# Kernel optimization log

Measured on AMD Instinct MI355X. Metric: run time of the kernel, lower is better.

## Reference

```python
import jax, jax.numpy as jnp
import numpy as np

N_LOW, N_HIGH = 5000, 50000
E_LH, E_HH = 200000, 400000


def _gatv2(xs, xd, src, dst, Wl, bl, Wr, br, att, bias, n_dst):
    """PyG GATv2Conv with aggr='mean', concat heads. att: [H, C]."""
    H, C = att.shape
    hl = (xs @ Wl + bl).reshape(-1, H, C)   # source transform (messages)
    hr = (xd @ Wr + br).reshape(-1, H, C)   # target transform
    z = jax.nn.leaky_relu(hl[src] + hr[dst], 0.2)        # [E, H, C]
    logit = jnp.einsum('ehc,hc->eh', z, att)             # [E, H]
    m = jax.lax.stop_gradient(jax.ops.segment_max(logit, dst, num_segments=n_dst))
    ex = jnp.exp(logit - m[dst])
    s = jax.ops.segment_sum(ex, dst, num_segments=n_dst)
    alpha = ex / (s[dst] + 1e-16)                        # edge softmax per dst, per head
    msg = hl[src] * alpha[..., None]                     # [E, H, C]
    out = jax.ops.segment_sum(msg, dst, num_segments=n_dst)
    cnt = jax.ops.segment_sum(jnp.ones(dst.shape, xs.dtype), dst, num_segments=n_dst)
    out = out / jnp.maximum(cnt, 1.0)[:, None, None]     # aggr='mean'
    return out.reshape(n_dst, H * C) + bias


def _bn(x, g, b):
    mu = x.mean(0)
    var = x.var(0)
    return (x - mu) * jax.lax.rsqrt(var + 1e-5) * g + b


def setup_inputs() -> dict:
    key = jax.random.key(0)
    it = iter(jax.random.split(key, 64))
    def nk():
        return next(it)
    def glorot(shape):
        s = np.sqrt(2.0 / (shape[0] + shape[-1])).astype(np.float32)
        return jax.random.normal(nk(), shape, jnp.float32) * s
    inp = {}
    inp['xl'] = jax.random.normal(nk(), (N_LOW, 125), jnp.float32)
    inp['xh'] = jax.random.normal(nk(), (N_HIGH, 1), jnp.float32)
    inp['zstd'] = jax.random.normal(nk(), (N_HIGH, 1), jnp.float32)
    inp['si_lh'] = jax.random.randint(nk(), (E_LH,), 0, N_LOW, jnp.int32)
    inp['di_lh'] = jax.random.randint(nk(), (E_LH,), 0, N_HIGH, jnp.int32)
    inp['si_hh'] = jax.random.randint(nk(), (E_HH,), 0, N_HIGH, jnp.int32)
    inp['di_hh'] = jax.random.randint(nk(), (E_HH,), 0, N_HIGH, jnp.int32)
    def gat(pfx, fs, fd, H, C):
        inp[pfx + '_Wl'] = glorot((fs, H * C)); inp[pfx + '_bl'] = jnp.zeros((H * C,), jnp.float32)
        inp[pfx + '_Wr'] = glorot((fd, H * C)); inp[pfx + '_br'] = jnp.zeros((H * C,), jnp.float32)
        inp[pfx + '_att'] = glorot((H, C)); inp[pfx + '_b'] = jnp.zeros((H * C,), jnp.float32)
    gat('d', 125, 1, 1, 256)
    gat('p1', 257, 257, 4, 64)
    gat('p2', 256, 256, 4, 64)
    gat('p3', 256, 256, 1, 64)
    for pfx, dim in [('bn0', 257), ('bn1', 256), ('bn2', 256), ('bn3', 64)]:
        inp[pfx + '_g'] = jnp.ones((dim,), jnp.float32)
        inp[pfx + '_b'] = jnp.zeros((dim,), jnp.float32)
    inp['pr_W1'] = glorot((64, 64)); inp['pr_b1'] = jnp.zeros((64,), jnp.float32)
    inp['pr_W2'] = glorot((64, 1)); inp['pr_b2'] = jnp.zeros((1,), jnp.float32)
    return inp


def reference(xl, xh, zstd, si_lh, di_lh, si_hh, di_hh,
              d_Wl, d_bl, d_Wr, d_br, d_att, d_b,
              p1_Wl, p1_bl, p1_Wr, p1_br, p1_att, p1_b,
              p2_Wl, p2_bl, p2_Wr, p2_br, p2_att, p2_b,
              p3_Wl, p3_bl, p3_Wr, p3_br, p3_att, p3_b,
              bn0_g, bn0_b, bn1_g, bn1_b, bn2_g, bn2_b, bn3_g, bn3_b,
              pr_W1, pr_b1, pr_W2, pr_b2):
    n_high = xh.shape[0]
    # downscaler: bipartite GATv2 (low -> high), heads=1, no self loops
    enc = _gatv2(xl, xh, si_lh, di_lh, d_Wl, d_bl, d_Wr, d_br, d_att, d_b, n_high)
    x = jnp.concatenate([zstd, enc], axis=-1)            # [N_HIGH, 257]
    # high-within-high edges with self loops (add_self_loops=True)
    loop = jnp.arange(n_high, dtype=si_hh.dtype)
    src = jnp.concatenate([si_hh, loop])
    dst = jnp.concatenate([di_hh, loop])
    x = _bn(x, bn0_g, bn0_b)
    x = _gatv2(x, x, src, dst, p1_Wl, p1_bl, p1_Wr, p1_br, p1_att, p1_b, n_high)
    x = jax.nn.relu(_bn(x, bn1_g, bn1_b))
    x = _gatv2(x, x, src, dst, p2_Wl, p2_bl, p2_Wr, p2_br, p2_att, p2_b, n_high)
    x = jax.nn.relu(_bn(x, bn2_g, bn2_b))
    x = _gatv2(x, x, src, dst, p3_Wl, p3_bl, p3_Wr, p3_br, p3_att, p3_b, n_high)
    x = jax.nn.relu(_bn(x, bn3_g, bn3_b))
    # predictor MLP
    y = jax.nn.relu(x @ pr_W1 + pr_b1) @ pr_W2 + pr_b2   # [N_HIGH, 1]
    return y
```

## Files before the change

kernel.cpp:

```cpp
#include <hip/hip_runtime.h>
#include <math.h>

#define DEV __device__ __forceinline__

static const int N_LOW = 5000, N_HIGH = 50000, E_LH = 200000, E_HH = 400000;
static const int E2 = E_HH + N_HIGH;
static const int ETOT = E_LH + E2;
static const int RBLK = 2048;

typedef __attribute__((ext_vector_type(8))) short bf16x8;
typedef __attribute__((ext_vector_type(4))) float f32x4;
typedef __attribute__((ext_vector_type(8))) unsigned short u16x8;
typedef unsigned short u16;

DEV short f2bf(float v) {
    unsigned u = __float_as_uint(v);
    u += 0x7FFFu + ((u >> 16) & 1u);
    return (short)(u >> 16);
}
DEV float bf2f(u16 u) { return __uint_as_float(((unsigned)u) << 16); }

template <int VPL> struct RawTT { using T = u16; };
template <> struct RawTT<4> { using T = ushort4; };

template <bool RELU, bool BF16OUT, bool WIDE>
DEV void gemm_body(const bf16x8* __restrict__ Af, const bf16x8* __restrict__ Bf,
                   const float* __restrict__ bias, float* __restrict__ C,
                   int M, int N, int nkt) {
    const int l = threadIdx.x & 63;
    const int w = threadIdx.x >> 6;
    const int nt0 = WIDE ? w * 4 : blockIdx.x * 4;
    const int mt0 = WIDE ? blockIdx.y * 2 : blockIdx.y * 8 + w * 2;
    f32x4 acc[2][4];
#pragma unroll
    for (int i = 0; i < 2; i++)
#pragma unroll
        for (int j = 0; j < 4; j++) acc[i][j] = (f32x4){0.f, 0.f, 0.f, 0.f};
    const bf16x8* a0p = Af + (size_t)mt0 * nkt * 64 + l;
    const bf16x8* a1p = a0p + (size_t)nkt * 64;
    const bf16x8* bp = Bf + (size_t)nt0 * nkt * 64 + l;
    for (int kt = 0; kt < nkt; kt++) {
        bf16x8 a0 = a0p[kt * 64];
        bf16x8 a1 = a1p[kt * 64];
        bf16x8 b0 = bp[kt * 64];
        bf16x8 b1 = bp[(size_t)(nkt + kt) * 64];
        bf16x8 b2 = bp[(size_t)(2 * nkt + kt) * 64];
        bf16x8 b3 = bp[(size_t)(3 * nkt + kt) * 64];
        acc[0][0] = __builtin_amdgcn_mfma_f32_16x16x32_bf16(a0, b0, acc[0][0], 0, 0, 0);
        acc[0][1] = __builtin_amdgcn_mfma_f32_16x16x32_bf16(a0, b1, acc[0][1], 0, 0, 0);
        acc[0][2] = __builtin_amdgcn_mfma_f32_16x16x32_bf16(a0, b2, acc[0][2], 0, 0, 0);
        acc[0][3] = __builtin_amdgcn_mfma_f32_16x16x32_bf16(a0, b3, acc[0][3], 0, 0, 0);
        acc[1][0] = __builtin_amdgcn_mfma_f32_16x16x32_bf16(a1, b0, acc[1][0], 0, 0, 0);
        acc[1][1] = __builtin_amdgcn_mfma_f32_16x16x32_bf16(a1, b1, acc[1][1], 0, 0, 0);
        acc[1][2] = __builtin_amdgcn_mfma_f32_16x16x32_bf16(a1, b2, acc[1][2], 0, 0, 0);
        acc[1][3] = __builtin_amdgcn_mfma_f32_16x16x32_bf16(a1, b3, acc[1][3], 0, 0, 0);
    }
    const int colb = nt0 * 16 + (l & 15);
    const int rsub = (l >> 4) * 4;
#pragma unroll
    for (int mi = 0; mi < 2; mi++) {
        int rowb = (mt0 + mi) * 16 + rsub;
#pragma unroll
        for (int r = 0; r < 4; r++) {
            int row = rowb + r;
            if (row >= M) continue;
#pragma unroll
            for (int n = 0; n < 4; n++) {
                int col = colb + n * 16;
                float v = acc[mi][n][r] + bias[col];
                if (RELU) v = fmaxf(v, 0.f);
                if (BF16OUT)
                    ((u16*)C)[(size_t)row * N + col] = (u16)f2bf(v);
                else
                    C[(size_t)row * N + col] = v;
            }
        }
    }
}

template <bool RELU, bool BF16OUT, bool WIDE>
__global__ __launch_bounds__(256) void gemm_mfma(
    const bf16x8* __restrict__ Af, const bf16x8* __restrict__ Bf,
    const float* __restrict__ bias, float* __restrict__ C,
    int M, int N, int nkt) {
    gemm_body<RELU, BF16OUT, WIDE>(Af, Bf, bias, C, M, N, nkt);
}

template <bool WIDE>
__global__ __launch_bounds__(256) void gemm_mfma2(
    const bf16x8* __restrict__ Af,
    const bf16x8* __restrict__ Bf0, const bf16x8* __restrict__ Bf1,
    const float* __restrict__ bias0, const float* __restrict__ bias1,
    float* __restrict__ C0, float* __restrict__ C1,
    int M, int N, int nkt) {
    if (blockIdx.z == 0)
        gemm_body<false, true, WIDE>(Af, Bf0, bias0, C0, M, N, nkt);
    else
        gemm_body<false, true, WIDE>(Af, Bf1, bias1, C1, M, N, nkt);
}

template <bool RELU>
__global__ __launch_bounds__(256) void bn_frag(
    const u16* __restrict__ x, int Nrows, int F, int STR, int SS,
    const float* __restrict__ sums,
    const float* __restrict__ g, const float* __restrict__ b,
    bf16x8* __restrict__ Af, int nmt, int nkt) {
    int total = nmt * nkt * 64;
    for (int idx = blockIdx.x * blockDim.x + threadIdx.x; idx < total;
         idx += gridDim.x * blockDim.x) {
        int mt = idx / (nkt * 64);
        int rem = idx - mt * (nkt * 64);
        int kt = rem >> 6, l = rem & 63;
        int row = mt * 16 + (l & 15);
        int colb = kt * 32 + (l >> 4) * 8;
        bf16x8 o;
#pragma unroll
        for (int j = 0; j < 8; j++) {
            int col = colb + j;
            float v = 0.f;
            if (row < Nrows && col < F) {
                float mu = sums[col] / Nrows;
                float var = sums[SS + col] / Nrows - mu * mu;
                float istd = rsqrtf(fmaxf(var, 0.f) + 1e-5f);
                v = (bf2f(x[(size_t)row * STR + col]) - mu) * istd * g[col] + b[col];
                if (RELU) v = fmaxf(v, 0.f);
            }
            o[j] = f2bf(v);
        }
        Af[idx] = o;
    }
}

__global__ __launch_bounds__(256) void cast_frag(
    const float* __restrict__ x, int Nrows, int F,
    bf16x8* __restrict__ Af, int nmt, int nkt) {
    int total = nmt * nkt * 64;
    for (int idx = blockIdx.x * blockDim.x + threadIdx.x; idx < total;
         idx += gridDim.x * blockDim.x) {
        int mt = idx / (nkt * 64);
        int rem = idx - mt * (nkt * 64);
        int kt = rem >> 6, l = rem & 63;
        int row = mt * 16 + (l & 15);
        int colb = kt * 32 + (l >> 4) * 8;
        bf16x8 o;
#pragma unroll
        for (int j = 0; j < 8; j++) {
            int col = colb + j;
            o[j] = (row < Nrows && col < F) ? f2bf(x[(size_t)row * F + col]) : (short)0;
        }
        Af[idx] = o;
    }
}

struct WtJobs {
    const float* W[8];
    bf16x8* out[8];
    int K[8], Nn[8], nnt[8], nkt[8];
};
__global__ __launch_bounds__(256) void wt_frag_all(WtJobs jobs) {
    const int job = blockIdx.y;
    const float* W = jobs.W[job];
    bf16x8* Bf = jobs.out[job];
    const int K = jobs.K[job], N = jobs.Nn[job];
    const int nkt = jobs.nkt[job];
    int total = jobs.nnt[job] * nkt * 64;
    for (int idx = blockIdx.x * blockDim.x + threadIdx.x; idx < total;
         idx += gridDim.x * blockDim.x) {
        int nt = idx / (nkt * 64);
        int rem = idx - nt * (nkt * 64);
        int kt = rem >> 6, l = rem & 63;
        int col = nt * 16 + (l & 15);
        int kb = kt * 32 + (l >> 4) * 8;
        bf16x8 o;
#pragma unroll
        for (int j = 0; j < 8; j++) {
            int k = kb + j;
            o[j] = (k < K && col < N) ? f2bf(W[(size_t)k * N + col]) : (short)0;
        }
        Bf[idx] = o;
    }
}

__global__ __launch_bounds__(256) void hist_all(
    const int* __restrict__ di_lh, const int* __restrict__ di_hh,
    int* __restrict__ cnt) {
    for (int i = blockIdx.x * blockDim.x + threadIdx.x; i < ETOT;
         i += gridDim.x * blockDim.x) {
        if (i < E_LH) {
            atomicAdd(&cnt[di_lh[i]], 1);
        } else {
            int j = i - E_LH;
            int d = (j < E_HH) ? di_hh[j] : (j - E_HH);
            atomicAdd(&cnt[N_HIGH + d], 1);
        }
    }
}

__global__ __launch_bounds__(256) void scan_partial(
    const int* __restrict__ cnt, int* __restrict__ off,
    int* __restrict__ bsum, int n) {
    __shared__ int s[256];
    const int t = threadIdx.x;
    const int base = blockIdx.x * 1024 + t * 4;
    int v0 = (base < n) ? cnt[base] : 0;
    int v1 = (base + 1 < n) ? cnt[base + 1] : 0;
    int v2 = (base + 2 < n) ? cnt[base + 2] : 0;
    int v3 = (base + 3 < n) ? cnt[base + 3] : 0;
    int tsum = v0 + v1 + v2 + v3;
    s[t] = tsum;
    __syncthreads();
    for (int step = 1; step < 256; step <<= 1) {
        int q = (t >= step) ? s[t - step] : 0;
        __syncthreads();
        s[t] += q;
        __syncthreads();
    }
    int excl = s[t] - tsum;
    if (base < n) off[base] = excl;
    if (base + 1 < n) off[base + 1] = excl + v0;
    if (base + 2 < n) off[base + 2] = excl + v0 + v1;
    if (base + 3 < n) off[base + 3] = excl + v0 + v1 + v2;
    if (t == 255) bsum[blockIdx.x] = s[255];
}

__global__ __launch_bounds__(256) void scan_bsums(
    int* __restrict__ bsum, int nb, int* __restrict__ off, int n) {
    __shared__ int s[256];
    const int t = threadIdx.x;
    int v = (t < nb) ? bsum[t] : 0;
    s[t] = v;
    __syncthreads();
    for (int step = 1; step < 256; step <<= 1) {
        int q = (t >= step) ? s[t - step] : 0;
        __syncthreads();
        s[t] += q;
        __syncthreads();
    }
    if (t < nb) bsum[t] = s[t] - v;
    if (t == 255) off[n] = s[255];
}

__global__ __launch_bounds__(256) void scan_add(
    int* __restrict__ off, const int* __restrict__ bsum, int n) {
    int b = blockIdx.x;
    int add = bsum[b];
    int base = b * 1024;
    int end = base + 1024 < n ? base + 1024 : n;
    for (int i = base + threadIdx.x; i < end; i += 256) off[i] += add;
}

__global__ __launch_bounds__(256) void scatter_all(
    const int* __restrict__ si_lh, const int* __restrict__ di_lh,
    const int* __restrict__ si_hh, const int* __restrict__ di_hh,
    int* __restrict__ cur, int* __restrict__ csr) {
    for (int i = blockIdx.x * blockDim.x + threadIdx.x; i < ETOT;
         i += gridDim.x * blockDim.x) {
        int d, s, bucket;
        if (i < E_LH) {
            d = di_lh[i]; s = si_lh[i]; bucket = d;
        } else {
            int j = i - E_LH;
            if (j < E_HH) { d = di_hh[j]; s = si_hh[j]; }
            else { d = s = j - E_HH; }
            bucket = N_HIGH + d;
        }
        int p = atomicAdd(&cur[bucket], 1);
        csr[p] = s;
    }
}

template <int H, int C, bool HR_ONFLY>
__global__ __launch_bounds__(256) void gat_gather(
    const u16* __restrict__ hl, const u16* __restrict__ hr,
    const float* __restrict__ xh, const float* __restrict__ Wr,
    const float* __restrict__ br,
    const int* __restrict__ rowptr, const int* __restrict__ csr_src,
    const float* __restrict__ att, const float* __restrict__ bias,
    u16* __restrict__ out, int outStride, int outOfs, int Ndst,
    const float* __restrict__ col0) {
    constexpr int HC = H * C;
    constexpr int VPL = HC / 64;
    constexpr int LPH = C / VPL;
    using RawT = typename RawTT<VPL>::T;
    int w = blockIdx.x * (blockDim.x >> 6) + (threadIdx.x >> 6);
    if (w >= Ndst) return;
    const int l = threadIdx.x & 63;

    float hrv[VPL], attv[VPL];
    if constexpr (HR_ONFLY) {
        static_assert(!HR_ONFLY || VPL == 4, "onfly assumes VPL==4");
        float xv = xh[w];
        float4 wr = *reinterpret_cast<const float4*>(Wr + l * 4);
        float4 bb = *reinterpret_cast<const float4*>(br + l * 4);
        hrv[0] = fmaf(xv, wr.x, bb.x); hrv[1] = fmaf(xv, wr.y, bb.y);
        hrv[2] = fmaf(xv, wr.z, bb.z); hrv[3] = fmaf(xv, wr.w, bb.w);
        float4 u = *reinterpret_cast<const float4*>(att + l * 4);
        attv[0] = u.x; attv[1] = u.y; attv[2] = u.z; attv[3] = u.w;
    } else if constexpr (VPL == 4) {
        ushort4 t = *(reinterpret_cast<const ushort4*>(hr + (size_t)w * HC) + l);
        hrv[0] = bf2f(t.x); hrv[1] = bf2f(t.y); hrv[2] = bf2f(t.z); hrv[3] = bf2f(t.w);
        float4 u = *reinterpret_cast<const float4*>(att + l * 4);
        attv[0] = u.x; attv[1] = u.y; attv[2] = u.z; attv[3] = u.w;
    } else {
#pragma unroll
        for (int j = 0; j < VPL; j++) {
            hrv[j] = bf2f(hr[(size_t)w * HC + l * VPL + j]);
            attv[j] = att[l * VPL + j];
        }
    }

    const int e0 = rowptr[w], e1 = rowptr[w + 1];
    float m = -3.4e38f, s = 0.f;
    float acc[VPL] = {};

    auto ldraw = [&](int sv) -> RawT {
        if constexpr (VPL == 4)
            return *(reinterpret_cast<const ushort4*>(hl + (size_t)sv * HC) + l);
        else
            return hl[(size_t)sv * HC + l];
    };
    auto proc = [&](RawT t) {
        float hlv[VPL];
        if constexpr (VPL == 4) {
            hlv[0] = bf2f(t.x); hlv[1] = bf2f(t.y);
            hlv[2] = bf2f(t.z); hlv[3] = bf2f(t.w);
        } else {
            hlv[0] = bf2f(t);
        }
        float v = 0.f;
#pragma unroll
        for (int j = 0; j < VPL; j++) {
            float z = hlv[j] + hrv[j];
            v = fmaf(fmaxf(z, 0.2f * z), attv[j], v);
        }
#pragma unroll
        for (int t2 = 1; t2 < LPH; t2 <<= 1) v += __shfl_xor(v, t2, 64);
        float d = v - m;
        bool up = d > 0.f;
        float ef = __expf(-fabsf(d));
        float sc = up ? ef : 1.f;
        float p  = up ? 1.f : ef;
        m = up ? v : m;
        s = fmaf(s, sc, p);
#pragma unroll
        for (int j = 0; j < VPL; j++) acc[j] = fmaf(acc[j], sc, p * hlv[j]);
    };

    int e = e0;
    for (; e + 3 < e1; e += 4) {
        int sv0 = csr_src[e];
        int sv1 = csr_src[e + 1];
        int sv2 = csr_src[e + 2];
        int sv3 = csr_src[e + 3];
        RawT t0 = ldraw(sv0);
        RawT t1 = ldraw(sv1);
        RawT t2 = ldraw(sv2);
        RawT t3 = ldraw(sv3);
        proc(t0); proc(t1); proc(t2); proc(t3);
    }
    for (; e < e1; e++) {
        RawT t = ldraw(csr_src[e]);
        proc(t);
    }

    float inv = 1.f / (s + 1e-16f);
    float dnorm = inv / fmaxf((float)(e1 - e0), 1.f);
    if constexpr (VPL == 4) {
        if (((outOfs | outStride) & 3) == 0) {
            ushort4 o;
            o.x = (u16)f2bf(acc[0] * dnorm + bias[l * 4 + 0]);
            o.y = (u16)f2bf(acc[1] * dnorm + bias[l * 4 + 1]);
            o.z = (u16)f2bf(acc[2] * dnorm + bias[l * 4 + 2]);
            o.w = (u16)f2bf(acc[3] * dnorm + bias[l * 4 + 3]);
            *(reinterpret_cast<ushort4*>(out + (size_t)w * outStride + outOfs) + l) = o;
        } else {
#pragma unroll
            for (int j = 0; j < 4; j++)
                out[(size_t)w * outStride + outOfs + l * 4 + j] =
                    (u16)f2bf(acc[j] * dnorm + bias[l * 4 + j]);
        }
    } else {
#pragma unroll
        for (int j = 0; j < VPL; j++)
            out[(size_t)w * outStride + outOfs + l * VPL + j] =
                (u16)f2bf(acc[j] * dnorm + bias[l * VPL + j]);
    }
    if (col0 && l == 0) out[(size_t)w * outStride] = (u16)f2bf(col0[w]);
}

template <int NC, int RPB>
__global__ __launch_bounds__(256) void bn_partial3(
    const u16* __restrict__ x, int Nrows, float* __restrict__ partials) {
    constexpr int STR = NC * 8;
    constexpr int NSTAT = 2 * NC * 8;
    const int t = threadIdx.x;
    const int b = blockIdx.x;
    __shared__ float l1[NC * RPB * 8];
    __shared__ float l2[NC * RPB * 8];
    float s1[8] = {}, s2[8] = {};
    if (t < NC * RPB) {
        const int rg = t / NC, cg = t - (t / NC) * NC;
        for (int r = b * RPB + rg; r < Nrows; r += RBLK * RPB) {
            u16x8 p = *reinterpret_cast<const u16x8*>(x + (size_t)r * STR + cg * 8);
#pragma unroll
            for (int j = 0; j < 8; j++) {
                float v = bf2f(p[j]);
                s1[j] += v; s2[j] += v * v;
            }
        }
#pragma unroll
        for (int j = 0; j < 8; j++) {
            l1[t * 8 + j] = s1[j];
            l2[t * 8 + j] = s2[j];
        }
    }
    __syncthreads();
    if (t < NC) {
        float a[8] = {}, c[8] = {};
#pragma unroll
        for (int rg = 0; rg < RPB; rg++)
#pragma unroll
            for (int j = 0; j < 8; j++) {
                a[j] += l1[(rg * NC + t) * 8 + j];
                c[j] += l2[(rg * NC + t) * 8 + j];
            }
#pragma unroll
        for (int j = 0; j < 8; j++) {
            partials[(size_t)b * NSTAT + t * 8 + j] = a[j];
            partials[(size_t)b * NSTAT + NC * 8 + t * 8 + j] = c[j];
        }
    }
}

__global__ __launch_bounds__(256) void bn_reduce2(
    const float* __restrict__ partials, int nstat, float* __restrict__ bsum) {
    const int sl = threadIdx.x & 63, ch = threadIdx.x >> 6;
    const int s = blockIdx.x * 64 + sl;
    const int b0 = blockIdx.y * (RBLK / 32);
    float v = 0.f;
    if (s < nstat) {
        for (int b = b0 + ch; b < b0 + RBLK / 32; b += 4)
            v += partials[(size_t)b * nstat + s];
    }
    __shared__ float l[256];
    l[threadIdx.x] = v;
    __syncthreads();
    if (ch == 0 && s < nstat)
        atomicAdd(&bsum[s], l[sl] + l[sl + 64] + l[sl + 128] + l[sl + 192]);
}

__global__ __launch_bounds__(256) void dot_w2(const float* __restrict__ hid,
                                              const float* __restrict__ W2,
                                              const float* __restrict__ b2,
                                              float* __restrict__ y, int N) {
    int w = blockIdx.x * (blockDim.x >> 6) + (threadIdx.x >> 6);
    int l = threadIdx.x & 63;
    if (w >= N) return;
    float v = hid[(size_t)w * 64 + l] * W2[l];
#pragma unroll
    for (int m = 1; m < 64; m <<= 1) v += __shfl_xor(v, m, 64);
    if (l == 0) y[w] = v + b2[0];
}

extern "C" void kernel_launch(void* const* d_in, const int* in_sizes, int n_in,
                              void* d_out, int out_size, void* d_ws, size_t ws_size,
                              hipStream_t stream) {
    const float* xl   = (const float*)d_in[0];
    const float* xh   = (const float*)d_in[1];
    const float* zstd = (const float*)d_in[2];
    const int* si_lh  = (const int*)d_in[3];
    const int* di_lh  = (const int*)d_in[4];
    const int* si_hh  = (const int*)d_in[5];
    const int* di_hh  = (const int*)d_in[6];
    int a = 7;
    const float *d_Wl = (const float*)d_in[a++], *d_bl = (const float*)d_in[a++],
                *d_Wr = (const float*)d_in[a++], *d_br = (const float*)d_in[a++],
                *d_att = (const float*)d_in[a++], *d_b = (const float*)d_in[a++];
    const float *p1_Wl = (const float*)d_in[a++], *p1_bl = (const float*)d_in[a++],
                *p1_Wr = (const float*)d_in[a++], *p1_br = (const float*)d_in[a++],
                *p1_att = (const float*)d_in[a++], *p1_b = (const float*)d_in[a++];
    const float *p2_Wl = (const float*)d_in[a++], *p2_bl = (const float*)d_in[a++],
                *p2_Wr = (const float*)d_in[a++], *p2_br = (const float*)d_in[a++],
                *p2_att = (const float*)d_in[a++], *p2_b = (const float*)d_in[a++];
    const float *p3_Wl = (const float*)d_in[a++], *p3_bl = (const float*)d_in[a++],
                *p3_Wr = (const float*)d_in[a++], *p3_br = (const float*)d_in[a++],
                *p3_att = (const float*)d_in[a++], *p3_b = (const float*)d_in[a++];
    const float *bn0_g = (const float*)d_in[a++], *bn0_b = (const float*)d_in[a++],
                *bn1_g = (const float*)d_in[a++], *bn1_b = (const float*)d_in[a++],
                *bn2_g = (const float*)d_in[a++], *bn2_b = (const float*)d_in[a++],
                *bn3_g = (const float*)d_in[a++], *bn3_b = (const float*)d_in[a++];
    const float *pr_W1 = (const float*)d_in[a++], *pr_b1 = (const float*)d_in[a++],
                *pr_W2 = (const float*)d_in[a++], *pr_b2 = (const float*)d_in[a++];
    float* y = (float*)d_out;

    const int N = N_HIGH;
    const int NMT = 3125;
    const int NB2 = (2 * N + 1023) / 1024;
    float* ws = (float*)d_ws;
    float* xA = ws;
    float* xB = xA + (size_t)N * 257;
    float* hl = xB + (size_t)N * 256;
    float* hr = hl + (size_t)N * 256;
    bf16x8* xl_f = (bf16x8*)(hr + (size_t)N * 256);
    bf16x8* wf_d   = xl_f + 320 * 4 * 64;
    bf16x8* wf_p1l = wf_d + 16 * 4 * 64;
    bf16x8* wf_p1r = wf_p1l + 16 * 9 * 64;
    bf16x8* wf_p2l = wf_p1r + 16 * 9 * 64;
    bf16x8* wf_p2r = wf_p2l + 16 * 8 * 64;
    bf16x8* wf_p3l = wf_p2r + 16 * 8 * 64;
    bf16x8* wf_p3r = wf_p3l + 4 * 8 * 64;
    bf16x8* wf_pr1 = wf_p3r + 4 * 8 * 64;
    float* bsum = (float*)(wf_pr1 + 4 * 2 * 64);
    int* bscan  = (int*)(bsum + 544);
    int* cnt    = bscan + 256;
    int* off    = cnt + 2 * N;
    int* cur    = off + 2 * N + 1;
    int* csr    = cur + 2 * N;
    size_t need = (size_t)((char*)(csr + ETOT) - (char*)ws);
    if (ws_size < need) return;
    bf16x8* AfB = (bf16x8*)xB;
    bf16x8* AfA = (bf16x8*)xA;
    u16* xA16 = (u16*)xA;
    u16* xB16 = (u16*)xB;
    u16* hl16 = (u16*)hl;
    u16* hr16 = (u16*)hr;
    float* partials = hr;
    int* rp_lh = off;
    int* rp_hh = off + N;

    dim3 blk(256);
    auto wgrid = [](int E) { return dim3((E + 3) / 4); };
    auto egrid = [](size_t total) {
        size_t g = (total + 255) / 256;
        return dim3((unsigned)(g > 2048 ? 2048 : g));
    };

    WtJobs jobs;
    jobs.W[0] = d_Wl;  jobs.out[0] = wf_d;   jobs.K[0] = 125; jobs.Nn[0] = 256; jobs.nnt[0] = 16; jobs.nkt[0] = 4;
    jobs.W[1] = p1_Wl; jobs.out[1] = wf_p1l; jobs.K[1] = 257; jobs.Nn[1] = 256; jobs.nnt[1] = 16; jobs.nkt[1] = 9;
    jobs.W[2] = p1_Wr; jobs.out[2] = wf_p1r; jobs.K[2] = 257; jobs.Nn[2] = 256; jobs.nnt[2] = 16; jobs.nkt[2] = 9;
    jobs.W[3] = p2_Wl; jobs.out[3] = wf_p2l; jobs.K[3] = 256; jobs.Nn[3] = 256; jobs.nnt[3] = 16; jobs.nkt[3] = 8;
    jobs.W[4] = p2_Wr; jobs.out[4] = wf_p2r; jobs.K[4] = 256; jobs.Nn[4] = 256; jobs.nnt[4] = 16; jobs.nkt[4] = 8;
    jobs.W[5] = p3_Wl; jobs.out[5] = wf_p3l; jobs.K[5] = 256; jobs.Nn[5] = 64;  jobs.nnt[5] = 4;  jobs.nkt[5] = 8;
    jobs.W[6] = p3_Wr; jobs.out[6] = wf_p3r; jobs.K[6] = 256; jobs.Nn[6] = 64;  jobs.nnt[6] = 4;  jobs.nkt[6] = 8;
    jobs.W[7] = pr_W1; jobs.out[7] = wf_pr1; jobs.K[7] = 64;  jobs.Nn[7] = 64;  jobs.nnt[7] = 4;  jobs.nkt[7] = 2;
    wt_frag_all<<<dim3(36, 8), blk, 0, stream>>>(jobs);
    cast_frag<<<dim3(320), blk, 0, stream>>>(xl, N_LOW, 125, xl_f, 320, 4);

    hipMemsetAsync(cnt, 0, 2 * (size_t)N * sizeof(int), stream);
    hist_all<<<egrid(ETOT), blk, 0, stream>>>(di_lh, di_hh, cnt);
    scan_partial<<<dim3(NB2), blk, 0, stream>>>(cnt, off, bscan, 2 * N);
    scan_bsums<<<dim3(1), blk, 0, stream>>>(bscan, NB2, off, 2 * N);
    scan_add<<<dim3(NB2), blk, 0, stream>>>(off, bscan, 2 * N);
    hipMemcpyAsync(cur, off, 2 * (size_t)N * sizeof(int), hipMemcpyDeviceToDevice, stream);
    scatter_all<<<egrid(ETOT), blk, 0, stream>>>(si_lh, di_lh, si_hh, di_hh, cur, csr);

    gemm_mfma<false, true, true><<<dim3(1, 157), blk, 0, stream>>>(xl_f, wf_d, d_bl, hl, N_LOW, 256, 4);
    gat_gather<1, 256, true><<<wgrid(N), blk, 0, stream>>>(
        hl16, nullptr, xh, d_Wr, d_br, rp_lh, csr, d_att, d_b, xA16, 264, 1, N, zstd);

    hipMemsetAsync(bsum, 0, 528 * sizeof(float), stream);
    bn_partial3<33, 7><<<dim3(RBLK), blk, 0, stream>>>(xA16, N, partials);
    bn_reduce2<<<dim3(9, 32), blk, 0, stream>>>(partials, 528, bsum);
    bn_frag<false><<<dim3(2048), blk, 0, stream>>>(xA16, N, 257, 264, 264, bsum, bn0_g, bn0_b, AfB, NMT, 9);

    gemm_mfma2<true><<<dim3(1, 1563, 2), blk, 0, stream>>>(AfB, wf_p1l, wf_p1r, p1_bl, p1_br, hl, hr, N, 256, 9);
    gat_gather<4, 64, false><<<wgrid(N), blk, 0, stream>>>(
        hl16, hr16, nullptr, nullptr, nullptr, rp_hh, csr, p1_att, p1_b, xB16, 256, 0, N, nullptr);
    hipMemsetAsync(bsum, 0, 512 * sizeof(float), stream);
    bn_partial3<32, 8><<<dim3(RBLK), blk, 0, stream>>>(xB16, N, partials);
    bn_reduce2<<<dim3(8, 32), blk, 0, stream>>>(partials, 512, bsum);
    bn_frag<true><<<dim3(2048), blk, 0, stream>>>(xB16, N, 256, 256, 256, bsum, bn1_g, bn1_b, AfA, NMT, 8);

    gemm_mfma2<true><<<dim3(1, 1563, 2), blk, 0, stream>>>(AfA, wf_p2l, wf_p2r, p2_bl, p2_br, hl, hr, N, 256, 8);
    gat_gather<4, 64, false><<<wgrid(N), blk, 0, stream>>>(
        hl16, hr16, nullptr, nullptr, nullptr, rp_hh, csr, p2_att, p2_b, xA16, 256, 0, N, nullptr);
    hipMemsetAsync(bsum, 0, 512 * sizeof(float), stream);
    bn_partial3<32, 8><<<dim3(RBLK), blk, 0, stream>>>(xA16, N, partials);
    bn_reduce2<<<dim3(8, 32), blk, 0, stream>>>(partials, 512, bsum);
    bn_frag<true><<<dim3(2048), blk, 0, stream>>>(xA16, N, 256, 256, 256, bsum, bn2_g, bn2_b, AfB, NMT, 8);

    gemm_mfma2<false><<<dim3(1, 391, 2), blk, 0, stream>>>(AfB, wf_p3l, wf_p3r, p3_bl, p3_br, hl, hr, N, 64, 8);
    gat_gather<1, 64, false><<<wgrid(N), blk, 0, stream>>>(
        hl16, hr16, nullptr, nullptr, nullptr, rp_hh, csr, p3_att, p3_b, xB16, 64, 0, N, nullptr);
    hipMemsetAsync(bsum, 0, 128 * sizeof(float), stream);
    bn_partial3<8, 32><<<dim3(RBLK), blk, 0, stream>>>(xB16, N, partials);
    bn_reduce2<<<dim3(2, 32), blk, 0, stream>>>(partials, 128, bsum);
    bn_frag<true><<<dim3(2048), blk, 0, stream>>>(xB16, N, 64, 64, 64, bsum, bn3_g, bn3_b, AfA, NMT, 2);

    gemm_mfma<true, false, false><<<dim3(1, 391), blk, 0, stream>>>(AfA, wf_pr1, pr_b1, hl, N, 64, 2);
    dot_w2<<<wgrid(N), blk, 0, stream>>>(hl, pr_W2, pr_b2, y, N);
}
```

Baseline: 514.6 us.

## Fuse predictor head, merge memsets and cast job, vectorize GAT gather math

Folds the final relu-MLP second layer into the MFMA GEMM epilogue with shuffle reductions, which removes the dot_w2 kernel and the round trip of the hidden activations. Merges the xl cast into the weight-fragment job kernel and replaces five memsets with one by giving each BN stage its own sum buffer. Rewrites the gather inner loop to use packed float2 math and exp2 with log2e-prescaled attention. The saving comes mostly from fewer launches and somewhat lighter gather ALU work. Reducing the rows in the epilogue with shuffles may add some cost there.

```diff
diff --git a/kernel.cpp b/kernel.cpp
--- a/kernel.cpp
+++ b/kernel.cpp
@@ -7,9 +7,11 @@
 static const int E2 = E_HH + N_HIGH;
 static const int ETOT = E_LH + E2;
 static const int RBLK = 2048;
+#define LOG2E 1.44269504088896f
 
 typedef __attribute__((ext_vector_type(8))) short bf16x8;
 typedef __attribute__((ext_vector_type(4))) float f32x4;
+typedef __attribute__((ext_vector_type(2))) float f32x2;
 typedef __attribute__((ext_vector_type(8))) unsigned short u16x8;
 typedef unsigned short u16;
 
@@ -21,7 +23,7 @@
 DEV float bf2f(u16 u) { return __uint_as_float(((unsigned)u) << 16); }
 
 template <int VPL> struct RawTT { using T = u16; };
-template <> struct RawTT<4> { using T = ushort4; };
+template <> struct RawTT<4> { using T = uint2; };
 
 template <bool RELU, bool BF16OUT, bool WIDE>
 DEV void gemm_body(const bf16x8* __restrict__ Af, const bf16x8* __restrict__ Bf,
@@ -99,6 +101,66 @@
         gemm_body<false, true, WIDE>(Af, Bf1, bias1, C1, M, N, nkt);
 }
 
+__global__ __launch_bounds__(256) void gemm_pred(
+    const bf16x8* __restrict__ Af, const bf16x8* __restrict__ Bf,
+    const float* __restrict__ bias, const float* __restrict__ W2,
+    const float* __restrict__ b2, float* __restrict__ y, int M, int nkt) {
+    const int l = threadIdx.x & 63;
+    const int w = threadIdx.x >> 6;
+    const int mt0 = blockIdx.y * 8 + w * 2;
+    f32x4 acc[2][4];
+#pragma unroll
+    for (int i = 0; i < 2; i++)
+#pragma unroll
+        for (int j = 0; j < 4; j++) acc[i][j] = (f32x4){0.f, 0.f, 0.f, 0.f};
+    const bf16x8* a0p = Af + (size_t)mt0 * nkt * 64 + l;
+    const bf16x8* a1p = a0p + (size_t)nkt * 64;
+    const bf16x8* bp = Bf + l;
+    for (int kt = 0; kt < nkt; kt++) {
+        bf16x8 a0 = a0p[kt * 64];
+        bf16x8 a1 = a1p[kt * 64];
+        bf16x8 b0 = bp[kt * 64];
+        bf16x8 b1 = bp[(size_t)(nkt + kt) * 64];
+        bf16x8 b2v = bp[(size_t)(2 * nkt + kt) * 64];
+        bf16x8 b3 = bp[(size_t)(3 * nkt + kt) * 64];
+        acc[0][0] = __builtin_amdgcn_mfma_f32_16x16x32_bf16(a0, b0, acc[0][0], 0, 0, 0);
+        acc[0][1] = __builtin_amdgcn_mfma_f32_16x16x32_bf16(a0, b1, acc[0][1], 0, 0, 0);
+        acc[0][2] = __builtin_amdgcn_mfma_f32_16x16x32_bf16(a0, b2v, acc[0][2], 0, 0, 0);
+        acc[0][3] = __builtin_amdgcn_mfma_f32_16x16x32_bf16(a0, b3, acc[0][3], 0, 0, 0);
+        acc[1][0] = __builtin_amdgcn_mfma_f32_16x16x32_bf16(a1, b0, acc[1][0], 0, 0, 0);
+        acc[1][1] = __builtin_amdgcn_mfma_f32_16x16x32_bf16(a1, b1, acc[1][1], 0, 0, 0);
+        acc[1][2] = __builtin_amdgcn_mfma_f32_16x16x32_bf16(a1, b2v, acc[1][2], 0, 0, 0);
+        acc[1][3] = __builtin_amdgcn_mfma_f32_16x16x32_bf16(a1, b3, acc[1][3], 0, 0, 0);
+    }
+    const int colb = l & 15;
+    const int rsub = (l >> 4) * 4;
+    float biasv[4], w2v[4];
+#pragma unroll
+    for (int n = 0; n < 4; n++) {
+        biasv[n] = bias[colb + n * 16];
+        w2v[n] = W2[colb + n * 16];
+    }
+    const float b2s = b2[0];
+#pragma unroll
+    for (int mi = 0; mi < 2; mi++) {
+#pragma unroll
+        for (int r = 0; r < 4; r++) {
+            int row = (mt0 + mi) * 16 + rsub + r;
+            float t = 0.f;
+#pragma unroll
+            for (int n = 0; n < 4; n++) {
+                float v = fmaxf(acc[mi][n][r] + biasv[n], 0.f);
+                t = fmaf(v, w2v[n], t);
+            }
+            t += __shfl_xor(t, 1, 64);
+            t += __shfl_xor(t, 2, 64);
+            t += __shfl_xor(t, 4, 64);
+            t += __shfl_xor(t, 8, 64);
+            if ((l & 15) == 0 && row < M) y[row] = t + b2s;
+        }
+    }
+}
+
 template <bool RELU>
 __global__ __launch_bounds__(256) void bn_frag(
     const u16* __restrict__ x, int Nrows, int F, int STR, int SS,
@@ -131,31 +193,10 @@
     }
 }
 
-__global__ __launch_bounds__(256) void cast_frag(
-    const float* __restrict__ x, int Nrows, int F,
-    bf16x8* __restrict__ Af, int nmt, int nkt) {
-    int total = nmt * nkt * 64;
-    for (int idx = blockIdx.x * blockDim.x + threadIdx.x; idx < total;
-         idx += gridDim.x * blockDim.x) {
-        int mt = idx / (nkt * 64);
-        int rem = idx - mt * (nkt * 64);
-        int kt = rem >> 6, l = rem & 63;
-        int row = mt * 16 + (l & 15);
-        int colb = kt * 32 + (l >> 4) * 8;
-        bf16x8 o;
-#pragma unroll
-        for (int j = 0; j < 8; j++) {
-            int col = colb + j;
-            o[j] = (row < Nrows && col < F) ? f2bf(x[(size_t)row * F + col]) : (short)0;
-        }
-        Af[idx] = o;
-    }
-}
-
 struct WtJobs {
-    const float* W[8];
-    bf16x8* out[8];
-    int K[8], Nn[8], nnt[8], nkt[8];
+    const float* W[9];
+    bf16x8* out[9];
+    int K[9], Nn[9], nnt[9], nkt[9], isA[9];
 };
 __global__ __launch_bounds__(256) void wt_frag_all(WtJobs jobs) {
     const int job = blockIdx.y;
@@ -163,19 +204,30 @@
     bf16x8* Bf = jobs.out[job];
     const int K = jobs.K[job], N = jobs.Nn[job];
     const int nkt = jobs.nkt[job];
+    const bool isA = jobs.isA[job] != 0;
     int total = jobs.nnt[job] * nkt * 64;
     for (int idx = blockIdx.x * blockDim.x + threadIdx.x; idx < total;
          idx += gridDim.x * blockDim.x) {
         int nt = idx / (nkt * 64);
         int rem = idx - nt * (nkt * 64);
         int kt = rem >> 6, l = rem & 63;
-        int col = nt * 16 + (l & 15);
-        int kb = kt * 32 + (l >> 4) * 8;
         bf16x8 o;
-#pragma unroll
-        for (int j = 0; j < 8; j++) {
-            int k = kb + j;
-            o[j] = (k < K && col < N) ? f2bf(W[(size_t)k * N + col]) : (short)0;
+        if (!isA) {
+            int col = nt * 16 + (l & 15);
+            int kb = kt * 32 + (l >> 4) * 8;
+#pragma unroll
+            for (int j = 0; j < 8; j++) {
+                int k = kb + j;
+                o[j] = (k < K && col < N) ? f2bf(W[(size_t)k * N + col]) : (short)0;
+            }
+        } else {
+            int row = nt * 16 + (l & 15);
+            int colb = kt * 32 + (l >> 4) * 8;
+#pragma unroll
+            for (int j = 0; j < 8; j++) {
+                int col = colb + j;
+                o[j] = (row < N && col < K) ? f2bf(W[(size_t)row * K + col]) : (short)0;
+            }
         }
         Bf[idx] = o;
     }
@@ -286,81 +338,111 @@
     if (w >= Ndst) return;
     const int l = threadIdx.x & 63;
 
-    float hrv[VPL], attv[VPL];
-    if constexpr (HR_ONFLY) {
-        static_assert(!HR_ONFLY || VPL == 4, "onfly assumes VPL==4");
-        float xv = xh[w];
-        float4 wr = *reinterpret_cast<const float4*>(Wr + l * 4);
-        float4 bb = *reinterpret_cast<const float4*>(br + l * 4);
-        hrv[0] = fmaf(xv, wr.x, bb.x); hrv[1] = fmaf(xv, wr.y, bb.y);
-        hrv[2] = fmaf(xv, wr.z, bb.z); hrv[3] = fmaf(xv, wr.w, bb.w);
-        float4 u = *reinterpret_cast<const float4*>(att + l * 4);
-        attv[0] = u.x; attv[1] = u.y; attv[2] = u.z; attv[3] = u.w;
-    } else if constexpr (VPL == 4) {
-        ushort4 t = *(reinterpret_cast<const ushort4*>(hr + (size_t)w * HC) + l);
-        hrv[0] = bf2f(t.x); hrv[1] = bf2f(t.y); hrv[2] = bf2f(t.z); hrv[3] = bf2f(t.w);
-        float4 u = *reinterpret_cast<const float4*>(att + l * 4);
-        attv[0] = u.x; attv[1] = u.y; attv[2] = u.z; attv[3] = u.w;
-    } else {
-#pragma unroll
-        for (int j = 0; j < VPL; j++) {
-            hrv[j] = bf2f(hr[(size_t)w * HC + l * VPL + j]);
-            attv[j] = att[l * VPL + j];
-        }
-    }
-
     const int e0 = rowptr[w], e1 = rowptr[w + 1];
     float m = -3.4e38f, s = 0.f;
-    float acc[VPL] = {};
-
-    auto ldraw = [&](int sv) -> RawT {
-        if constexpr (VPL == 4)
-            return *(reinterpret_cast<const ushort4*>(hl + (size_t)sv * HC) + l);
-        else
-            return hl[(size_t)sv * HC + l];
-    };
-    auto proc = [&](RawT t) {
-        float hlv[VPL];
-        if constexpr (VPL == 4) {
-            hlv[0] = bf2f(t.x); hlv[1] = bf2f(t.y);
-            hlv[2] = bf2f(t.z); hlv[3] = bf2f(t.w);
+    float accout[VPL];
+
+    if constexpr (VPL == 4) {
+        f32x2 hr2[2], at2[2];
+        if constexpr (HR_ONFLY) {
+            float xv = xh[w];
+            float4 wr = *reinterpret_cast<const float4*>(Wr + l * 4);
+            float4 bb = *reinterpret_cast<const float4*>(br + l * 4);
+            hr2[0].x = fmaf(xv, wr.x, bb.x); hr2[0].y = fmaf(xv, wr.y, bb.y);
+            hr2[1].x = fmaf(xv, wr.z, bb.z); hr2[1].y = fmaf(xv, wr.w, bb.w);
         } else {
-            hlv[0] = bf2f(t);
-        }
-        float v = 0.f;
-#pragma unroll
-        for (int j = 0; j < VPL; j++) {
-            float z = hlv[j] + hrv[j];
-            v = fmaf(fmaxf(z, 0.2f * z), attv[j], v);
-        }
-#pragma unroll
-        for (int t2 = 1; t2 < LPH; t2 <<= 1) v += __shfl_xor(v, t2, 64);
-        float d = v - m;
-        bool up = d > 0.f;
-        float ef = __expf(-fabsf(d));
-        float sc = up ? ef : 1.f;
-        float p  = up ? 1.f : ef;
-        m = up ? v : m;
-        s = fmaf(s, sc, p);
-#pragma unroll
-        for (int j = 0; j < VPL; j++) acc[j] = fmaf(acc[j], sc, p * hlv[j]);
-    };
-
-    int e = e0;
-    for (; e + 3 < e1; e += 4) {
-        int sv0 = csr_src[e];
-        int sv1 = csr_src[e + 1];
-        int sv2 = csr_src[e + 2];
-        int sv3 = csr_src[e + 3];
-        RawT t0 = ldraw(sv0);
-        RawT t1 = ldraw(sv1);
-        RawT t2 = ldraw(sv2);
-        RawT t3 = ldraw(sv3);
-        proc(t0); proc(t1); proc(t2); proc(t3);
-    }
-    for (; e < e1; e++) {
-        RawT t = ldraw(csr_src[e]);
-        proc(t);
+            uint2 tt = *(reinterpret_cast<const uint2*>(hr + (size_t)w * HC) + l);
+            hr2[0].x = __uint_as_float(tt.x << 16);
+            hr2[0].y = __uint_as_float(tt.x & 0xFFFF0000u);
+            hr2[1].x = __uint_as_float(tt.y << 16);
+            hr2[1].y = __uint_as_float(tt.y & 0xFFFF0000u);
+        }
+        {
+            float4 u = *reinterpret_cast<const float4*>(att + l * 4);
+            at2[0].x = u.x * LOG2E; at2[0].y = u.y * LOG2E;
+            at2[1].x = u.z * LOG2E; at2[1].y = u.w * LOG2E;
+        }
+        f32x2 acc2[2] = {{0.f, 0.f}, {0.f, 0.f}};
+
+        auto proc = [&](uint2 tt) {
+            f32x2 h0, h1;
+            h0.x = __uint_as_float(tt.x << 16);
+            h0.y = __uint_as_float(tt.x & 0xFFFF0000u);
+            h1.x = __uint_as_float(tt.y << 16);
+            h1.y = __uint_as_float(tt.y & 0xFFFF0000u);
+            f32x2 z0 = h0 + hr2[0];
+            f32x2 z1 = h1 + hr2[1];
+            z0 = __builtin_elementwise_max(z0, z0 * 0.2f);
+            z1 = __builtin_elementwise_max(z1, z1 * 0.2f);
+            f32x2 v2 = z0 * at2[0];
+            v2 = __builtin_elementwise_fma(z1, at2[1], v2);
+            float v = v2.x + v2.y;
+#pragma unroll
+            for (int t2 = 1; t2 < LPH; t2 <<= 1) v += __shfl_xor(v, t2, 64);
+            float d = v - m;
+            bool up = d > 0.f;
+            float ef = exp2f(-fabsf(d));
+            float sc = up ? ef : 1.f;
+            float p  = up ? 1.f : ef;
+            m = up ? v : m;
+            s = fmaf(s, sc, p);
+            f32x2 sc2; sc2.x = sc; sc2.y = sc;
+            f32x2 p2;  p2.x = p;  p2.y = p;
+            acc2[0] = __builtin_elementwise_fma(acc2[0], sc2, h0 * p2);
+            acc2[1] = __builtin_elementwise_fma(acc2[1], sc2, h1 * p2);
+        };
+
+        int e = e0;
+        for (; e + 3 < e1; e += 4) {
+            int sv0 = csr_src[e];
+            int sv1 = csr_src[e + 1];
+            int sv2 = csr_src[e + 2];
+            int sv3 = csr_src[e + 3];
+            uint2 t0 = *(reinterpret_cast<const uint2*>(hl + (size_t)sv0 * HC) + l);
+            uint2 t1 = *(reinterpret_cast<const uint2*>(hl + (size_t)sv1 * HC) + l);
+            uint2 t2 = *(reinterpret_cast<const uint2*>(hl + (size_t)sv2 * HC) + l);
+            uint2 t3 = *(reinterpret_cast<const uint2*>(hl + (size_t)sv3 * HC) + l);
+            proc(t0); proc(t1); proc(t2); proc(t3);
+        }
+        for (; e < e1; e++) {
+            uint2 t = *(reinterpret_cast<const uint2*>(hl + (size_t)csr_src[e] * HC) + l);
+            proc(t);
+        }
+        accout[0] = acc2[0].x; accout[1] = acc2[0].y;
+        accout[2] = acc2[1].x; accout[3] = acc2[1].y;
+    } else {
+        float hrv = bf2f(hr[(size_t)w * HC + l]);
+        float attv = att[l] * LOG2E;
+        float acc = 0.f;
+        auto proc = [&](u16 t) {
+            float hlv = bf2f(t);
+            float z = hlv + hrv;
+            float v = fmaxf(z, 0.2f * z) * attv;
+#pragma unroll
+            for (int t2 = 1; t2 < LPH; t2 <<= 1) v += __shfl_xor(v, t2, 64);
+            float d = v - m;
+            bool up = d > 0.f;
+            float ef = exp2f(-fabsf(d));
+            float sc = up ? ef : 1.f;
+            float p  = up ? 1.f : ef;
+            m = up ? v : m;
+            s = fmaf(s, sc, p);
+            acc = fmaf(acc, sc, p * hlv);
+        };
+        int e = e0;
+        for (; e + 3 < e1; e += 4) {
+            int sv0 = csr_src[e];
+            int sv1 = csr_src[e + 1];
+            int sv2 = csr_src[e + 2];
+            int sv3 = csr_src[e + 3];
+            u16 t0 = hl[(size_t)sv0 * HC + l];
+            u16 t1 = hl[(size_t)sv1 * HC + l];
+            u16 t2 = hl[(size_t)sv2 * HC + l];
+            u16 t3 = hl[(size_t)sv3 * HC + l];
+            proc(t0); proc(t1); proc(t2); proc(t3);
+        }
+        for (; e < e1; e++) proc(hl[(size_t)csr_src[e] * HC + l]);
+        accout[0] = acc;
     }
 
     float inv = 1.f / (s + 1e-16f);
@@ -368,22 +450,20 @@
     if constexpr (VPL == 4) {
         if (((outOfs | outStride) & 3) == 0) {
             ushort4 o;
-            o.x = (u16)f2bf(acc[0] * dnorm + bias[l * 4 + 0]);
-            o.y = (u16)f2bf(acc[1] * dnorm + bias[l * 4 + 1]);
-            o.z = (u16)f2bf(acc[2] * dnorm + bias[l * 4 + 2]);
-            o.w = (u16)f2bf(acc[3] * dnorm + bias[l * 4 + 3]);
+            o.x = (u16)f2bf(accout[0] * dnorm + bias[l * 4 + 0]);
+            o.y = (u16)f2bf(accout[1] * dnorm + bias[l * 4 + 1]);
+            o.z = (u16)f2bf(accout[2] * dnorm + bias[l * 4 + 2]);
+            o.w = (u16)f2bf(accout[3] * dnorm + bias[l * 4 + 3]);
             *(reinterpret_cast<ushort4*>(out + (size_t)w * outStride + outOfs) + l) = o;
         } else {
 #pragma unroll
             for (int j = 0; j < 4; j++)
                 out[(size_t)w * outStride + outOfs + l * 4 + j] =
-                    (u16)f2bf(acc[j] * dnorm + bias[l * 4 + j]);
+                    (u16)f2bf(accout[j] * dnorm + bias[l * 4 + j]);
         }
     } else {
-#pragma unroll
-        for (int j = 0; j < VPL; j++)
-            out[(size_t)w * outStride + outOfs + l * VPL + j] =
-                (u16)f2bf(acc[j] * dnorm + bias[l * VPL + j]);
+        out[(size_t)w * outStride + outOfs + l] =
+            (u16)f2bf(accout[0] * dnorm + bias[l]);
     }
     if (col0 && l == 0) out[(size_t)w * outStride] = (u16)f2bf(col0[w]);
 }
@@ -447,19 +527,6 @@
     __syncthreads();
     if (ch == 0 && s < nstat)
         atomicAdd(&bsum[s], l[sl] + l[sl + 64] + l[sl + 128] + l[sl + 192]);
-}
-
-__global__ __launch_bounds__(256) void dot_w2(const float* __restrict__ hid,
-                                              const float* __restrict__ W2,
-                                              const float* __restrict__ b2,
-                                              float* __restrict__ y, int N) {
-    int w = blockIdx.x * (blockDim.x >> 6) + (threadIdx.x >> 6);
-    int l = threadIdx.x & 63;
-    if (w >= N) return;
-    float v = hid[(size_t)w * 64 + l] * W2[l];
-#pragma unroll
-    for (int m = 1; m < 64; m <<= 1) v += __shfl_xor(v, m, 64);
-    if (l == 0) y[w] = v + b2[0];
 }
 
 extern "C" void kernel_launch(void* const* d_in, const int* in_sizes, int n_in,
@@ -511,7 +578,7 @@
     bf16x8* wf_p3r = wf_p3l + 4 * 8 * 64;
     bf16x8* wf_pr1 = wf_p3r + 4 * 8 * 64;
     float* bsum = (float*)(wf_pr1 + 4 * 2 * 64);
-    int* bscan  = (int*)(bsum + 544);
+    int* bscan  = (int*)(bsum + 4 * 544);
     int* cnt    = bscan + 256;
     int* off    = cnt + 2 * N;
     int* cur    = off + 2 * N + 1;
@@ -536,18 +603,19 @@
     };
 
     WtJobs jobs;
-    jobs.W[0] = d_Wl;  jobs.out[0] = wf_d;   jobs.K[0] = 125; jobs.Nn[0] = 256; jobs.nnt[0] = 16; jobs.nkt[0] = 4;
-    jobs.W[1] = p1_Wl; jobs.out[1] = wf_p1l; jobs.K[1] = 257; jobs.Nn[1] = 256; jobs.nnt[1] = 16; jobs.nkt[1] = 9;
-    jobs.W[2] = p1_Wr; jobs.out[2] = wf_p1r; jobs.K[2] = 257; jobs.Nn[2] = 256; jobs.nnt[2] = 16; jobs.nkt[2] = 9;
-    jobs.W[3] = p2_Wl; jobs.out[3] = wf_p2l; jobs.K[3] = 256; jobs.Nn[3] = 256; jobs.nnt[3] = 16; jobs.nkt[3] = 8;
-    jobs.W[4] = p2_Wr; jobs.out[4] = wf_p2r; jobs.K[4] = 256; jobs.Nn[4] = 256; jobs.nnt[4] = 16; jobs.nkt[4] = 8;
-    jobs.W[5] = p3_Wl; jobs.out[5] = wf_p3l; jobs.K[5] = 256; jobs.Nn[5] = 64;  jobs.nnt[5] = 4;  jobs.nkt[5] = 8;
-    jobs.W[6] = p3_Wr; jobs.out[6] = wf_p3r; jobs.K[6] = 256; jobs.Nn[6] = 64;  jobs.nnt[6] = 4;  jobs.nkt[6] = 8;
-    jobs.W[7] = pr_W1; jobs.out[7] = wf_pr1; jobs.K[7] = 64;  jobs.Nn[7] = 64;  jobs.nnt[7] = 4;  jobs.nkt[7] = 2;
-    wt_frag_all<<<dim3(36, 8), blk, 0, stream>>>(jobs);
-    cast_frag<<<dim3(320), blk, 0, stream>>>(xl, N_LOW, 125, xl_f, 320, 4);
-
-    hipMemsetAsync(cnt, 0, 2 * (size_t)N * sizeof(int), stream);
+    jobs.W[0] = d_Wl;  jobs.out[0] = wf_d;   jobs.K[0] = 125; jobs.Nn[0] = 256; jobs.nnt[0] = 16; jobs.nkt[0] = 4; jobs.isA[0] = 0;
+    jobs.W[1] = p1_Wl; jobs.out[1] = wf_p1l; jobs.K[1] = 257; jobs.Nn[1] = 256; jobs.nnt[1] = 16; jobs.nkt[1] = 9; jobs.isA[1] = 0;
+    jobs.W[2] = p1_Wr; jobs.out[2] = wf_p1r; jobs.K[2] = 257; jobs.Nn[2] = 256; jobs.nnt[2] = 16; jobs.nkt[2] = 9; jobs.isA[2] = 0;
+    jobs.W[3] = p2_Wl; jobs.out[3] = wf_p2l; jobs.K[3] = 256; jobs.Nn[3] = 256; jobs.nnt[3] = 16; jobs.nkt[3] = 8; jobs.isA[3] = 0;
+    jobs.W[4] = p2_Wr; jobs.out[4] = wf_p2r; jobs.K[4] = 256; jobs.Nn[4] = 256; jobs.nnt[4] = 16; jobs.nkt[4] = 8; jobs.isA[4] = 0;
+    jobs.W[5] = p3_Wl; jobs.out[5] = wf_p3l; jobs.K[5] = 256; jobs.Nn[5] = 64;  jobs.nnt[5] = 4;  jobs.nkt[5] = 8; jobs.isA[5] = 0;
+    jobs.W[6] = p3_Wr; jobs.out[6] = wf_p3r; jobs.K[6] = 256; jobs.Nn[6] = 64;  jobs.nnt[6] = 4;  jobs.nkt[6] = 8; jobs.isA[6] = 0;
+    jobs.W[7] = pr_W1; jobs.out[7] = wf_pr1; jobs.K[7] = 64;  jobs.Nn[7] = 64;  jobs.nnt[7] = 4;  jobs.nkt[7] = 2; jobs.isA[7] = 0;
+    jobs.W[8] = xl;    jobs.out[8] = xl_f;   jobs.K[8] = 125; jobs.Nn[8] = N_LOW; jobs.nnt[8] = 320; jobs.nkt[8] = 4; jobs.isA[8] = 1;
+    wt_frag_all<<<dim3(36, 9), blk, 0, stream>>>(jobs);
+
+    hipMemsetAsync(bsum, 0, (4 * 544 + 256 + 2 * (size_t)N) * sizeof(float), stream);
+
     hist_all<<<egrid(ETOT), blk, 0, stream>>>(di_lh, di_hh, cnt);
     scan_partial<<<dim3(NB2), blk, 0, stream>>>(cnt, off, bscan, 2 * N);
     scan_bsums<<<dim3(1), blk, 0, stream>>>(bscan, NB2, off, 2 * N);
@@ -559,7 +627,6 @@
     gat_gather<1, 256, true><<<wgrid(N), blk, 0, stream>>>(
         hl16, nullptr, xh, d_Wr, d_br, rp_lh, csr, d_att, d_b, xA16, 264, 1, N, zstd);
 
-    hipMemsetAsync(bsum, 0, 528 * sizeof(float), stream);
     bn_partial3<33, 7><<<dim3(RBLK), blk, 0, stream>>>(xA16, N, partials);
     bn_reduce2<<<dim3(9, 32), blk, 0, stream>>>(partials, 528, bsum);
     bn_frag<false><<<dim3(2048), blk, 0, stream>>>(xA16, N, 257, 264, 264, bsum, bn0_g, bn0_b, AfB, NMT, 9);
@@ -567,27 +634,23 @@
     gemm_mfma2<true><<<dim3(1, 1563, 2), blk, 0, stream>>>(AfB, wf_p1l, wf_p1r, p1_bl, p1_br, hl, hr, N, 256, 9);
     gat_gather<4, 64, false><<<wgrid(N), blk, 0, stream>>>(
         hl16, hr16, nullptr, nullptr, nullptr, rp_hh, csr, p1_att, p1_b, xB16, 256, 0, N, nullptr);
-    hipMemsetAsync(bsum, 0, 512 * sizeof(float), stream);
     bn_partial3<32, 8><<<dim3(RBLK), blk, 0, stream>>>(xB16, N, partials);
-    bn_reduce2<<<dim3(8, 32), blk, 0, stream>>>(partials, 512, bsum);
-    bn_frag<true><<<dim3(2048), blk, 0, stream>>>(xB16, N, 256, 256, 256, bsum, bn1_g, bn1_b, AfA, NMT, 8);
+    bn_reduce2<<<dim3(8, 32), blk, 0, stream>>>(partials, 512, bsum + 544);
+    bn_frag<true><<<dim3(2048), blk, 0, stream>>>(xB16, N, 256, 256, 256, bsum + 544, bn1_g, bn1_b, AfA, NMT, 8);
 
     gemm_mfma2<true><<<dim3(1, 1563, 2), blk, 0, stream>>>(AfA, wf_p2l, wf_p2r, p2_bl, p2_br, hl, hr, N, 256, 8);
     gat_gather<4, 64, false><<<wgrid(N), blk, 0, stream>>>(
         hl16, hr16, nullptr, nullptr, nullptr, rp_hh, csr, p2_att, p2_b, xA16, 256, 0, N, nullptr);
-    hipMemsetAsync(bsum, 0, 512 * sizeof(float), stream);
     bn_partial3<32, 8><<<dim3(RBLK), blk, 0, stream>>>(xA16, N, partials);
-    bn_reduce2<<<dim3(8, 32), blk, 0, stream>>>(partials, 512, bsum);
-    bn_frag<true><<<dim3(2048), blk, 0, stream>>>(xA16, N, 256, 256, 256, bsum, bn2_g, bn2_b, AfB, NMT, 8);
+    bn_reduce2<<<dim3(8, 32), blk, 0, stream>>>(partials, 512, bsum + 2 * 544);
+    bn_frag<true><<<dim3(2048), blk, 0, stream>>>(xA16, N, 256, 256, 256, bsum + 2 * 544, bn2_g, bn2_b, AfB, NMT, 8);
 
     gemm_mfma2<false><<<dim3(1, 391, 2), blk, 0, stream>>>(AfB, wf_p3l, wf_p3r, p3_bl, p3_br, hl, hr, N, 64, 8);
     gat_gather<1, 64, false><<<wgrid(N), blk, 0, stream>>>(
         hl16, hr16, nullptr, nullptr, nullptr, rp_hh, csr, p3_att, p3_b, xB16, 64, 0, N, nullptr);
-    hipMemsetAsync(bsum, 0, 128 * sizeof(float), stream);
     bn_partial3<8, 32><<<dim3(RBLK), blk, 0, stream>>>(xB16, N, partials);
-    bn_reduce2<<<dim3(2, 32), blk, 0, stream>>>(partials, 128, bsum);
-    bn_frag<true><<<dim3(2048), blk, 0, stream>>>(xB16, N, 64, 64, 64, bsum, bn3_g, bn3_b, AfA, NMT, 2);
-
-    gemm_mfma<true, false, false><<<dim3(1, 391), blk, 0, stream>>>(AfA, wf_pr1, pr_b1, hl, N, 64, 2);
-    dot_w2<<<wgrid(N), blk, 0, stream>>>(hl, pr_W2, pr_b2, y, N);
-}
+    bn_reduce2<<<dim3(2, 32), blk, 0, stream>>>(partials, 128, bsum + 3 * 544);
+    bn_frag<true><<<dim3(2048), blk, 0, stream>>>(xB16, N, 64, 64, 64, bsum + 3 * 544, bn3_g, bn3_b, AfA, NMT, 2);
+
+    gemm_pred<<<dim3(1, 391), blk, 0, stream>>>(AfA, wf_pr1, pr_b1, pr_W2, pr_b2, y, N, 2);
+}
```

Result: no change. 509.0 us (-1.1%).
